# Kernel tuning notes

Measured on AMD Instinct MI355X. Metric: run time of the kernel, lower is better.

Reference implementation:

```python
import jax, jax.numpy as jnp
import numpy as np
import math

G = 128          # graphs per batch
N_PER = 512      # nodes per graph (equal-size, contiguous layout)
N = G * N_PER    # 65536 nodes
DEG = 16
E = N * DEG      # 1,048,576 edges
IN_C, HID, OUT_C = 100, 128, 2
RATIO = 0.8
EPS = 1e-5

K1 = int(math.ceil(RATIO * N_PER))  # 410
K2 = int(math.ceil(RATIO * K1))     # 328
K3 = int(math.ceil(RATIO * K2))     # 263


def gcn_conv(x, src, dst, emask, W, b):
    # GCNConv: linear, symmetric deg^-1/2 norm with self-loops, scatter-add
    xl = x @ W
    n = x.shape[0]
    w = emask.astype(x.dtype)
    deg = jnp.ones((n,), x.dtype).at[dst].add(w)      # +1 from self loop
    dinv = jax.lax.rsqrt(deg)
    coef = dinv[src] * dinv[dst] * w                  # [E]
    out = jnp.zeros_like(xl).at[dst].add(coef[:, None] * xl[src])
    out = out + (dinv * dinv)[:, None] * xl           # self-loop messages
    return out + b


def batch_norm(x, gamma, beta):
    # BatchNorm1d over node dim (training-mode batch statistics)
    mu = x.mean(0)
    var = x.var(0)
    return (x - mu) * jax.lax.rsqrt(var + EPS) * gamma + beta


def topk_pool(x, src, dst, emask, att, g, n, k):
    # TopKPooling: score = tanh(x@att/||att||), keep top-k per graph, gate features,
    # drop edges touching removed nodes (via validity mask).
    score = jnp.tanh((x @ att) / jnp.linalg.norm(att))
    _, idx = jax.lax.top_k(score.reshape(g, n), k)           # [g,k] local ids
    kept = (idx + (jnp.arange(g) * n)[:, None]).reshape(-1)   # global ids
    new_x = x[kept] * score[kept][:, None]
    old2new = jnp.full((g * n,), -1, jnp.int32).at[kept].set(
        jnp.arange(g * k, dtype=jnp.int32))
    s2, d2 = old2new[src], old2new[dst]
    valid = emask & (s2 >= 0) & (d2 >= 0)
    return new_x, jnp.maximum(s2, 0), jnp.maximum(d2, 0), valid


def readout(x, g, k):
    # [global_max_pool, global_mean_pool] over each graph's k nodes
    xr = x.reshape(g, k, -1)
    return jnp.concatenate([xr.max(1), xr.mean(1)], axis=1)   # [g, 2C]


def setup_inputs() -> dict:
    key = jax.random.key(0)
    ks = jax.random.split(key, 16)
    x = jax.random.normal(ks[0], (N, IN_C), jnp.float32)
    # within-graph random edges, then offset by graph id
    e_per = E // G
    local = jax.random.randint(ks[1], (2, G, e_per), 0, N_PER)
    edge_index = (local + (jnp.arange(G) * N_PER)[None, :, None]).reshape(2, E).astype(jnp.int32)
    batch = jnp.repeat(jnp.arange(G, dtype=jnp.int32), N_PER)

    def w(k, fi, fo):
        return jax.random.normal(k, (fi, fo), jnp.float32) * (1.0 / np.sqrt(fi))

    z = lambda c: jnp.zeros((c,), jnp.float32)
    o = lambda c: jnp.ones((c,), jnp.float32)
    return {
        'x': x, 'edge_index': edge_index, 'batch': batch,
        'Wp': w(ks[2], IN_C, 128), 'bp': z(128),
        'W1': w(ks[3], 128, HID), 'b1': z(HID), 'g1': o(HID), 'be1': z(HID),
        'att1': jax.random.normal(ks[4], (HID,), jnp.float32),
        'W2': w(ks[5], HID, HID), 'b2': z(HID), 'g2': o(HID), 'be2': z(HID),
        'att2': jax.random.normal(ks[6], (HID,), jnp.float32),
        'W3': w(ks[7], HID, HID), 'b3': z(HID), 'g3': o(HID), 'be3': z(HID),
        'att3': jax.random.normal(ks[8], (HID,), jnp.float32),
        'Wl1': w(ks[9], 2 * HID, HID), 'bl1': z(HID),
        'Wl2': w(ks[10], HID, OUT_C), 'bl2': z(OUT_C),
    }


def reference(x, edge_index, batch, Wp, bp, W1, b1, g1, be1, att1,
              W2, b2, g2, be2, att2, W3, b3, g3, be3, att3,
              Wl1, bl1, Wl2, bl2):
    src, dst = edge_index[0], edge_index[1]
    emask = jnp.ones((E,), bool)
    h = jax.nn.relu(x @ Wp + bp)

    h = jax.nn.relu(batch_norm(gcn_conv(h, src, dst, emask, W1, b1), g1, be1))
    h, src, dst, emask = topk_pool(h, src, dst, emask, att1, G, N_PER, K1)
    x1 = readout(h, G, K1)

    h = jax.nn.relu(batch_norm(gcn_conv(h, src, dst, emask, W2, b2), g2, be2))
    h, src, dst, emask = topk_pool(h, src, dst, emask, att2, G, K1, K2)
    x2 = readout(h, G, K2)

    h = jax.nn.relu(batch_norm(gcn_conv(h, src, dst, emask, W3, b3), g3, be3))
    h, src, dst, emask = topk_pool(h, src, dst, emask, att3, G, K2, K3)
    x3 = readout(h, G, K3)

    s = x1 + x2 + x3                       # [G, 2*HID]
    s = jax.nn.relu(s @ Wl1 + bl1)
    return s @ Wl2 + bl2                   # [G, OUT_C]
```

## Files before the change

### kernel.cpp

```cpp
#include <hip/hip_runtime.h>
#include <math.h>

#define G     128
#define NPER  512
#define NTOT  65536
#define E_TOT 1048576
#define EPG   8192
#define INC   100
#define HID   128
#define KP1   410
#define KP2   328
#define KP3   263

__global__ void init_kernel(short* __restrict__ cmap, float* __restrict__ sread,
                            float* __restrict__ bnpart) {
    int t = blockIdx.x * 256 + threadIdx.x;
    if (t < NTOT) cmap[t] = (short)(t & (NPER - 1));
    if (t < G * 256) sread[t] = 0.f;
    if (t < 3 * G * 256) bnpart[t] = 0.f;
}

__global__ __launch_bounds__(512, 2) void csr_build0(
    const int* __restrict__ src, const int* __restrict__ dst,
    unsigned short* __restrict__ csr_g, int* __restrict__ rowptr_g)
{
    __shared__ int cnt_s[NPER];
    __shared__ int rowptr_s[NPER + 1];
    __shared__ int wo_s[NPER];
    __shared__ int chunksum_s[9];

    const int g = blockIdx.x, tid = threadIdx.x, lane = tid & 63, wv = tid >> 6;
    const int ebase = g * EPG, obase = g * NPER;

    cnt_s[tid] = 0;
    __syncthreads();
    for (int e = tid; e < EPG; e += 512)
        atomicAdd(&cnt_s[dst[ebase + e] - obase], 1);
    __syncthreads();

    int v = cnt_s[tid], x = v;
#pragma unroll
    for (int d = 1; d < 64; d <<= 1) {
        int y = __shfl_up(x, d);
        if (lane >= d) x += y;
    }
    if (lane == 63) chunksum_s[wv] = x;
    __syncthreads();
    if (tid == 0) {
        int acc = 0;
#pragma unroll
        for (int k = 0; k < 8; ++k) { int t = chunksum_s[k]; chunksum_s[k] = acc; acc += t; }
    }
    __syncthreads();
    int excl = x - v + chunksum_s[wv];
    rowptr_s[tid] = excl; wo_s[tid] = excl;
    if (tid == 511) rowptr_s[512] = excl + v;
    __syncthreads();

    for (int i = tid; i <= NPER; i += 512) rowptr_g[g * 513 + i] = rowptr_s[i];
    for (int e = tid; e < EPG; e += 512) {
        int sl = src[ebase + e] - obase, dl = dst[ebase + e] - obase;
        int pos = atomicAdd(&wo_s[dl], 1);
        csr_g[g * EPG + pos] = (unsigned short)sl;
    }
}

__global__ __launch_bounds__(256, 2) void gemm_pre(
    const float* __restrict__ A, const float* __restrict__ W,
    const float* __restrict__ bias, float* __restrict__ out, int M)
{
    constexpr int K = INC, KC = 32;
    __shared__ float Ws[KC][128];
    __shared__ float As[KC][132];
    const int tid  = threadIdx.x;
    const int row0 = blockIdx.x * 128;
    const int r0 = (tid >> 4) * 8;
    const int c0 = (tid & 15) * 8;

    float acc[8][8];
#pragma unroll
    for (int i = 0; i < 8; ++i)
#pragma unroll
        for (int j = 0; j < 8; ++j) acc[i][j] = 0.f;

    for (int k0 = 0; k0 < K; k0 += KC) {
        const int kc  = (K - k0 < KC) ? (K - k0) : KC;
        const int nf4 = kc >> 2;

        for (int i = tid; i < kc * 32; i += 256) {
            int kk = i >> 5, c4 = i & 31;
            *((float4*)&Ws[kk][0] + c4) =
                *((const float4*)(W + (size_t)(k0 + kk) * 128) + c4);
        }
        for (int i = tid; i < nf4 * 128; i += 256) {
            int row = i / nf4, f4 = i - row * nf4;
            float4 v = *(const float4*)(A + (size_t)(row0 + row) * K + k0 + f4 * 4);
            As[f4 * 4 + 0][row] = v.x;
            As[f4 * 4 + 1][row] = v.y;
            As[f4 * 4 + 2][row] = v.z;
            As[f4 * 4 + 3][row] = v.w;
        }
        __syncthreads();

#pragma unroll 4
        for (int kk = 0; kk < kc; ++kk) {
            float4 b0 = *(const float4*)&Ws[kk][c0];
            float4 b1 = *(const float4*)&Ws[kk][c0 + 4];
            float4 a0 = *(const float4*)&As[kk][r0];
            float4 a1 = *(const float4*)&As[kk][r0 + 4];
            float a[8] = {a0.x, a0.y, a0.z, a0.w, a1.x, a1.y, a1.z, a1.w};
            float b[8] = {b0.x, b0.y, b0.z, b0.w, b1.x, b1.y, b1.z, b1.w};
#pragma unroll
            for (int i = 0; i < 8; ++i)
#pragma unroll
                for (int j = 0; j < 8; ++j)
                    acc[i][j] += a[i] * b[j];
        }
        __syncthreads();
    }

#pragma unroll
    for (int i = 0; i < 8; ++i) {
        int row = row0 + r0 + i;
        float o[8];
#pragma unroll
        for (int j = 0; j < 8; ++j)
            o[j] = fmaxf(acc[i][j] + bias[c0 + j], 0.f);
        float* po = out + (size_t)row * 128 + c0;
        *(float4*)po       = make_float4(o[0], o[1], o[2], o[3]);
        *(float4*)(po + 4) = make_float4(o[4], o[5], o[6], o[7]);
    }
}

template<int NCUR>
__global__ __launch_bounds__(256, 2) void gemm128(
    const float* __restrict__ A, const float* __restrict__ W,
    const int* __restrict__ rowptr_g, float* __restrict__ out)
{
    constexpr int KC = 32;
    __shared__ float Ws[2][KC][128];
    __shared__ float As[2][KC][132];
    __shared__ float dinv_ls[128];
    const int tid  = threadIdx.x;
    const int row0 = blockIdx.x * 128;
    const int r0 = (tid >> 4) * 8;
    const int c0 = (tid & 15) * 8;

    if (tid < 128) {
        int row = row0 + tid;
        int gg = row / NCUR, ll = row - gg * NCUR;
        const int* rp = rowptr_g + gg * 513 + ll;
        dinv_ls[tid] = rsqrtf((float)(rp[1] - rp[0] + 1));
    }

    const float4* W4 = (const float4*)W;

#pragma unroll
    for (int j = 0; j < 4; ++j) {
        int i = tid + j * 256;
        int kk = i >> 5, c4 = i & 31;
        *((float4*)&Ws[0][kk][0] + c4) = W4[kk * 32 + c4];
    }
#pragma unroll
    for (int j = 0; j < 4; ++j) {
        int i = tid + j * 256;
        int row = i >> 3, f4 = i & 7;
        float4 v = *(const float4*)(A + (size_t)(row0 + row) * 128 + f4 * 4);
        As[0][f4 * 4 + 0][row] = v.x;
        As[0][f4 * 4 + 1][row] = v.y;
        As[0][f4 * 4 + 2][row] = v.z;
        As[0][f4 * 4 + 3][row] = v.w;
    }
    __syncthreads();

    float acc[8][8];
#pragma unroll
    for (int i = 0; i < 8; ++i)
#pragma unroll
        for (int j = 0; j < 8; ++j) acc[i][j] = 0.f;

    int p = 0;
    for (int k0 = 0; k0 < 128; k0 += KC) {
        const int kn = k0 + KC;
        const bool has = kn < 128;

        float4 wreg[4], areg[4];
        if (has) {
#pragma unroll
            for (int j = 0; j < 4; ++j) {
                int i = tid + j * 256;
                int kk = i >> 5, c4 = i & 31;
                wreg[j] = W4[(kn + kk) * 32 + c4];
            }
#pragma unroll
            for (int j = 0; j < 4; ++j) {
                int i = tid + j * 256;
                int row = i >> 3, f4 = i & 7;
                areg[j] = *(const float4*)(A + (size_t)(row0 + row) * 128 + kn + f4 * 4);
            }
        }

#pragma unroll 4
        for (int kk = 0; kk < KC; ++kk) {
            float4 b0 = *(const float4*)&Ws[p][kk][c0];
            float4 b1 = *(const float4*)&Ws[p][kk][c0 + 4];
            float4 a0 = *(const float4*)&As[p][kk][r0];
            float4 a1 = *(const float4*)&As[p][kk][r0 + 4];
            float a[8] = {a0.x, a0.y, a0.z, a0.w, a1.x, a1.y, a1.z, a1.w};
            float b[8] = {b0.x, b0.y, b0.z, b0.w, b1.x, b1.y, b1.z, b1.w};
#pragma unroll
            for (int i = 0; i < 8; ++i)
#pragma unroll
                for (int j = 0; j < 8; ++j)
                    acc[i][j] += a[i] * b[j];
        }

        if (has) {
            int q = p ^ 1;
#pragma unroll
            for (int j = 0; j < 4; ++j) {
                int i = tid + j * 256;
                int kk = i >> 5, c4 = i & 31;
                *((float4*)&Ws[q][kk][0] + c4) = wreg[j];
            }
#pragma unroll
            for (int j = 0; j < 4; ++j) {
                int i = tid + j * 256;
                int row = i >> 3, f4 = i & 7;
                float4 v = areg[j];
                As[q][f4 * 4 + 0][row] = v.x;
                As[q][f4 * 4 + 1][row] = v.y;
                As[q][f4 * 4 + 2][row] = v.z;
                As[q][f4 * 4 + 3][row] = v.w;
            }
        }
        __syncthreads();
        p ^= 1;
    }

#pragma unroll
    for (int i = 0; i < 8; ++i) {
        int row = row0 + r0 + i;
        float dv = dinv_ls[r0 + i];
        float o[8];
#pragma unroll
        for (int j = 0; j < 8; ++j) o[j] = acc[i][j] * dv;
        float* po = out + (size_t)row * 128 + c0;
        *(float4*)po       = make_float4(o[0], o[1], o[2], o[3]);
        *(float4*)(po + 4) = make_float4(o[4], o[5], o[6], o[7]);
    }
}

template<int NCUR>
__global__ __launch_bounds__(256, 8) void gather_kernel(
    const float* __restrict__ xs, const unsigned short* __restrict__ csr_g,
    const int* __restrict__ rowptr_g, const float* __restrict__ bvec,
    float* __restrict__ out, float* __restrict__ bnpart)
{
    constexpr int CHUNK = (NCUR + 15) / 16;
    constexpr int CSRCAP = 1536;
    __shared__ int   rowptr_s[CHUNK + 1];
    __shared__ unsigned short csr_s[CSRCAP];
    __shared__ float red_s[512];

    const int g = blockIdx.x, s = blockIdx.y;
    const int tid = threadIdx.x, lane = tid & 63, w = tid >> 6;
    const int nbase = g * NCUR;
    const int d0 = s * CHUNK;
    const int d1 = (d0 + CHUNK < NCUR) ? d0 + CHUNK : NCUR;
    const int len = d1 - d0;

    const int* rp = rowptr_g + g * 513 + d0;
    for (int i = tid; i <= len; i += 256) rowptr_s[i] = rp[i];
    __syncthreads();

    const int base = rowptr_s[0];
    int nume = rowptr_s[len] - base;
    if (nume > CSRCAP) nume = CSRCAP;
    const unsigned short* cg = csr_g + g * EPG + base;
    for (int i = tid; i < nume; i += 256) csr_s[i] = cg[i];
    __syncthreads();

    const float2* x2g = (const float2*)xs + (size_t)nbase * 64 + lane;
    float2* o2p = (float2*)out;
    const float2 b2 = ((const float2*)bvec)[lane];
    float2 sum = make_float2(0.f, 0.f), sq = make_float2(0.f, 0.f);

    for (int da = d0 + w; da < d1; da += 8) {
        const int db = da + 4;
        const bool hb = db < d1;
        const int ra = da - d0, rb = db - d0;
        const int ia = rowptr_s[ra] - base;
        const int na = rowptr_s[ra + 1] - rowptr_s[ra];
        const int ib = hb ? rowptr_s[rb] - base : 0;
        const int nbl = hb ? rowptr_s[rb + 1] - rowptr_s[rb] : 0;
        const float dva = rsqrtf((float)(na + 1));
        const float dvb = rsqrtf((float)(nbl + 1));

        float2 accA = x2g[(size_t)da * 64];
        float2 accB = make_float2(0.f, 0.f);
        if (hb) accB = x2g[(size_t)db * 64];

        const int nmin = na < nbl ? na : nbl;
#pragma unroll 2
        for (int t = 0; t < nmin; ++t) {
            int sa = csr_s[ia + t], sb = csr_s[ib + t];
            float2 va = x2g[(size_t)sa * 64];
            float2 vb = x2g[(size_t)sb * 64];
            accA.x += va.x; accA.y += va.y;
            accB.x += vb.x; accB.y += vb.y;
        }
#pragma unroll 4
        for (int t = nmin; t < na; ++t) {
            float2 va = x2g[(size_t)csr_s[ia + t] * 64];
            accA.x += va.x; accA.y += va.y;
        }
#pragma unroll 4
        for (int t = nmin; t < nbl; ++t) {
            float2 vb = x2g[(size_t)csr_s[ib + t] * 64];
            accB.x += vb.x; accB.y += vb.y;
        }

        float2 oA = make_float2(b2.x + dva * accA.x, b2.y + dva * accA.y);
        o2p[(size_t)(nbase + da) * 64 + lane] = oA;
        sum.x += oA.x; sum.y += oA.y;
        sq.x  += oA.x * oA.x; sq.y += oA.y * oA.y;
        if (hb) {
            float2 oB = make_float2(b2.x + dvb * accB.x, b2.y + dvb * accB.y);
            o2p[(size_t)(nbase + db) * 64 + lane] = oB;
            sum.x += oB.x; sum.y += oB.y;
            sq.x  += oB.x * oB.x; sq.y += oB.y * oB.y;
        }
    }

    float2* red2 = (float2*)red_s;
    red2[tid] = sum; __syncthreads();
    if (tid < 64) {
        float2 a = red2[tid], b_ = red2[tid + 64],
               c = red2[tid + 128], d_ = red2[tid + 192];
        atomicAdd(&bnpart[g * 256 + 2 * tid],     a.x + b_.x + c.x + d_.x);
        atomicAdd(&bnpart[g * 256 + 2 * tid + 1], a.y + b_.y + c.y + d_.y);
    }
    __syncthreads();
    red2[tid] = sq; __syncthreads();
    if (tid < 64) {
        float2 a = red2[tid], b_ = red2[tid + 64],
               c = red2[tid + 128], d_ = red2[tid + 192];
        atomicAdd(&bnpart[g * 256 + 128 + 2 * tid],     a.x + b_.x + c.x + d_.x);
        atomicAdd(&bnpart[g * 256 + 128 + 2 * tid + 1], a.y + b_.y + c.y + d_.y);
    }
}

__global__ __launch_bounds__(1024, 1) void bnfin_kernel(
    const float* __restrict__ bnpart, float n,
    const float* __restrict__ gamma, const float* __restrict__ beta,
    const float* __restrict__ att, float* __restrict__ coefs)
{
    __shared__ float ssum[8][128];
    __shared__ float ssq[8][128];
    __shared__ float r[128];
    const int t = threadIdx.x & 127, slice = threadIdx.x >> 7;
    float s = 0.f, q = 0.f;
    for (int g = slice; g < G; g += 8) {
        s += bnpart[g * 256 + t];
        q += bnpart[g * 256 + 128 + t];
    }
    ssum[slice][t] = s; ssq[slice][t] = q;
    if (threadIdx.x < 128) { float av = att[t]; r[t] = av * av; }
    __syncthreads();
    if (threadIdx.x < 128) {
        float S = 0.f, Q = 0.f;
#pragma unroll
        for (int k = 0; k < 8; ++k) { S += ssum[k][t]; Q += ssq[k][t]; }
        for (int st = 64; st > 0; st >>= 1) {
            if (t < st) r[t] += r[t + st];
            __syncthreads();
        }
        float norm = sqrtf(r[0]);
        float mu   = S / n;
        float var  = Q / n - mu * mu;
        float inv  = rsqrtf(var + 1e-5f);
        float a    = gamma[t] * inv;
        coefs[t]        = a;
        coefs[128 + t]  = beta[t] - mu * a;
        coefs[256 + t]  = att[t] / norm;
    }
}

template<int NCUR, int KK, bool BUILD>
__global__ __launch_bounds__(1024, 1) void pool_kernel(
    const float* __restrict__ gcn, const float* __restrict__ coefs,
    float* __restrict__ newx, short* __restrict__ cmap,
    float* __restrict__ sread,
    const int* __restrict__ src, const int* __restrict__ dst,
    unsigned short* __restrict__ csr_g, int* __restrict__ rowptr_g)
{
    __shared__ float score_s[NCUR];
    __shared__ unsigned long long key_s[NCUR];
    __shared__ short o2n_s[NCUR];
    __shared__ unsigned short n2o_s[KK];
    __shared__ short cmap_s[NPER];
    __shared__ float2 red2[1024];
    __shared__ int   cnt_s[512];
    __shared__ int   rowptr_s[513];
    __shared__ int   wo_s[512];
    __shared__ int   chunksum_s[9];

    const int g = blockIdx.x, tid = threadIdx.x, lane = tid & 63, w = tid >> 6;
    const int nb = g * NCUR;
    const int ebase = g * EPG, obase = g * NPER;
    const float a0 = coefs[lane],       a1 = coefs[64 + lane];
    const float c0 = coefs[128 + lane], c1 = coefs[192 + lane];
    const float t0 = coefs[256 + lane], t1 = coefs[320 + lane];

    for (int i = tid; i < NPER; i += 1024) cmap_s[i] = cmap[obase + i];

    for (int i = w; i < NCUR; i += 16) {
        const float* row = gcn + (size_t)(nb + i) * 128;
        float h0 = fmaxf(a0 * row[lane] + c0, 0.f);
        float h1 = fmaxf(a1 * row[64 + lane] + c1, 0.f);
        float p  = h0 * t0 + h1 * t1;
#pragma unroll
        for (int off = 32; off > 0; off >>= 1) p += __shfl_down(p, off);
        if (lane == 0) score_s[i] = tanhf(p);
    }
    __syncthreads();

    for (int i = tid; i < NCUR; i += 1024) {
        unsigned u   = __float_as_uint(score_s[i]);
        unsigned key = (u & 0x80000000u) ? ~u : (u | 0x80000000u);
        key_s[i] = ((unsigned long long)key << 32) |
                   (unsigned long long)(0xFFFFFFFFu - (unsigned)i);
    }
    __syncthreads();

    for (int i = tid; i < NCUR; i += 1024) {
        const unsigned long long ki = key_s[i];
        int r = 0;
#pragma unroll 8
        for (int j = 0; j < NCUR; ++j) r += (key_s[j] > ki) ? 1 : 0;
        o2n_s[i] = (r < KK) ? (short)r : (short)-1;
        if (r < KK) n2o_s[r] = (unsigned short)i;
    }
    __syncthreads();

    float mx0 = -1e30f, mx1 = -1e30f, sm0 = 0.f, sm1 = 0.f;
    for (int j2 = w; j2 < KK; j2 += 16) {
        int old = n2o_s[j2];
        float s = score_s[old];
        const float* row = gcn + (size_t)(nb + old) * 128;
        float h0 = fmaxf(a0 * row[lane] + c0, 0.f) * s;
        float h1 = fmaxf(a1 * row[64 + lane] + c1, 0.f) * s;
        float* orow = newx + (size_t)(g * KK + j2) * 128;
        orow[lane]      = h0;
        orow[64 + lane] = h1;
        mx0 = fmaxf(mx0, h0); mx1 = fmaxf(mx1, h1);
        sm0 += h0; sm1 += h1;
    }
    red2[tid] = make_float2(mx0, mx1);
    __syncthreads();
    if (tid < 64) {
        float m = -1e30f;
#pragma unroll
        for (int w2 = 0; w2 < 16; ++w2) m = fmaxf(m, red2[w2 * 64 + tid].x);
        sread[g * 256 + tid] += m;
    } else if (tid < 128) {
        int l = tid - 64;
        float m = -1e30f;
#pragma unroll
        for (int w2 = 0; w2 < 16; ++w2) m = fmaxf(m, red2[w2 * 64 + l].y);
        sread[g * 256 + tid] += m;
    }
    __syncthreads();
    red2[tid] = make_float2(sm0, sm1);
    __syncthreads();
    if (tid < 64) {
        float sm = 0.f;
#pragma unroll
        for (int w2 = 0; w2 < 16; ++w2) sm += red2[w2 * 64 + tid].x;
        sread[g * 256 + 128 + tid] += sm * (1.0f / KK);
    } else if (tid < 128) {
        int l = tid - 64;
        float sm = 0.f;
#pragma unroll
        for (int w2 = 0; w2 < 16; ++w2) sm += red2[w2 * 64 + l].y;
        sread[g * 256 + 128 + tid] += sm * (1.0f / KK);
    }

    for (int o = tid; o < NPER; o += 1024) {
        int m = cmap_s[o];
        short nm = (m >= 0) ? o2n_s[m] : (short)-1;
        cmap_s[o] = nm;
        cmap[obase + o] = nm;
    }

    if (!BUILD) return;
    __syncthreads();

    if (tid < 512) cnt_s[tid] = 0;
    __syncthreads();
    for (int e = tid; e < EPG; e += 1024) {
        int sl = cmap_s[src[ebase + e] - obase];
        int dl = cmap_s[dst[ebase + e] - obase];
        if ((sl | dl) >= 0) atomicAdd(&cnt_s[dl], 1);
    }
    __syncthreads();
    int v = 0, x = 0;
    if (tid < 512) {
        v = cnt_s[tid]; x = v;
#pragma unroll
        for (int d = 1; d < 64; d <<= 1) {
            int y = __shfl_up(x, d);
            if (lane >= d) x += y;
        }
        if (lane == 63) chunksum_s[w] = x;
    }
    __syncthreads();
    if (tid == 0) {
        int acc = 0;
#pragma unroll
        for (int k = 0; k < 8; ++k) { int t = chunksum_s[k]; chunksum_s[k] = acc; acc += t; }
    }
    __syncthreads();
    if (tid < 512) {
        int excl = x - v + chunksum_s[w];
        rowptr_s[tid] = excl; wo_s[tid] = excl;
        if (tid == 511) rowptr_s[512] = excl + v;
    }
    __syncthreads();
    for (int i = tid; i <= 512; i += 1024) rowptr_g[g * 513 + i] = rowptr_s[i];
    for (int e = tid; e < EPG; e += 1024) {
        int sl = cmap_s[src[ebase + e] - obase];
        int dl = cmap_s[dst[ebase + e] - obase];
        if ((sl | dl) >= 0) {
            int pos = atomicAdd(&wo_s[dl], 1);
            csr_g[g * EPG + pos] = (unsigned short)sl;
        }
    }
}

__global__ void final_kernel(const float* __restrict__ sread,
                             const float* __restrict__ Wl1,
                             const float* __restrict__ bl1,
                             const float* __restrict__ Wl2,
                             const float* __restrict__ bl2,
                             float* __restrict__ out)
{
    __shared__ float s_s[256];
    __shared__ float hid_s[128];
    int g = blockIdx.x, t = threadIdx.x;
    s_s[t]       = sread[g * 256 + t];
    s_s[128 + t] = sread[g * 256 + 128 + t];
    __syncthreads();
    float acc = bl1[t];
    for (int i = 0; i < 256; ++i) acc += s_s[i] * Wl1[i * 128 + t];
    hid_s[t] = fmaxf(acc, 0.f);
    __syncthreads();
    if (t < 2) {
        float o = bl2[t];
        for (int j = 0; j < 128; ++j) o += hid_s[j] * Wl2[j * 2 + t];
        out[g * 2 + t] = o;
    }
}

extern "C" void kernel_launch(void* const* d_in, const int* in_sizes, int n_in,
                              void* d_out, int out_size, void* d_ws, size_t ws_size,
                              hipStream_t stream)
{
    const float* x    = (const float*)d_in[0];
    const int*   ei   = (const int*)d_in[1];
    const float* Wp   = (const float*)d_in[3];
    const float* bp   = (const float*)d_in[4];
    const float* W1   = (const float*)d_in[5];
    const float* b1   = (const float*)d_in[6];
    const float* g1   = (const float*)d_in[7];
    const float* be1  = (const float*)d_in[8];
    const float* att1 = (const float*)d_in[9];
    const float* W2   = (const float*)d_in[10];
    const float* b2   = (const float*)d_in[11];
    const float* g2   = (const float*)d_in[12];
    const float* be2  = (const float*)d_in[13];
    const float* att2 = (const float*)d_in[14];
    const float* W3   = (const float*)d_in[15];
    const float* b3   = (const float*)d_in[16];
    const float* g3   = (const float*)d_in[17];
    const float* be3  = (const float*)d_in[18];
    const float* att3 = (const float*)d_in[19];
    const float* Wl1  = (const float*)d_in[20];
    const float* bl1  = (const float*)d_in[21];
    const float* Wl2  = (const float*)d_in[22];
    const float* bl2  = (const float*)d_in[23];
    float* out = (float*)d_out;

    const int* srcp = ei;
    const int* dstp = ei + E_TOT;

    char* ws = (char*)d_ws;
    float*          bufA   = (float*)ws;
    float*          bufB   = (float*)(ws + 33554432);
    unsigned short* csr    = (unsigned short*)(ws + 67108864);
    int*            rowptr = (int*)  (ws + 69206016);
    float*          bnpart = (float*)(ws + 69468672);
    short*          cmap   = (short*)(ws + 69861888);
    float*          sread  = (float*)(ws + 69992960);
    float*          coefs  = (float*)(ws + 70124032);

    float* bn0 = bnpart;
    float* bn1 = bnpart + G * 256;
    float* bn2 = bnpart + 2 * G * 256;

    init_kernel<<<384, 256, 0, stream>>>(cmap, sread, bnpart);
    csr_build0<<<G, 512, 0, stream>>>(srcp, dstp, csr, rowptr);

    gemm_pre<<<512, 256, 0, stream>>>(x, Wp, bp, bufA, NTOT);

    gemm128<NPER><<<512, 256, 0, stream>>>(bufA, W1, rowptr, bufB);
    gather_kernel<NPER><<<dim3(G, 16), 256, 0, stream>>>(bufB, csr, rowptr, b1, bufA, bn0);
    bnfin_kernel<<<1, 1024, 0, stream>>>(bn0, (float)NTOT, g1, be1, att1, coefs);
    pool_kernel<NPER, KP1, true><<<G, 1024, 0, stream>>>(
        bufA, coefs, bufB, cmap, sread, srcp, dstp, csr, rowptr);

    gemm128<KP1><<<410, 256, 0, stream>>>(bufB, W2, rowptr, bufA);
    gather_kernel<KP1><<<dim3(G, 16), 256, 0, stream>>>(bufA, csr, rowptr, b2, bufB, bn1);
    bnfin_kernel<<<1, 1024, 0, stream>>>(bn1, (float)(G * KP1), g2, be2, att2, coefs);
    pool_kernel<KP1, KP2, true><<<G, 1024, 0, stream>>>(
        bufB, coefs, bufA, cmap, sread, srcp, dstp, csr, rowptr);

    gemm128<KP2><<<328, 256, 0, stream>>>(bufA, W3, rowptr, bufB);
    gather_kernel<KP2><<<dim3(G, 16), 256, 0, stream>>>(bufB, csr, rowptr, b3, bufA, bn2);
    bnfin_kernel<<<1, 1024, 0, stream>>>(bn2, (float)(G * KP2), g3, be3, att3, coefs);
    pool_kernel<KP2, KP3, false><<<G, 1024, 0, stream>>>(
        bufA, coefs, bufB, cmap, sread, srcp, dstp, csr, rowptr);

    final_kernel<<<G, 128, 0, stream>>>(sread, Wl1, bl1, Wl2, bl2, out);
}
```

Baseline: 485.6 us.

## Split pool kernel into parallel score, select and gate kernels

Each per-graph pool kernel ran as 128 blocks of 1024 threads. It is now split into three kernels. The score and gating/readout kernels each launch 1024 smaller blocks to spread the memory-bound row reads across more CUs. Only the top-k ranking and CSR rebuild stay per-graph. The readout max and mean are accumulated with global atomics, the max using an order-preserving uint encoding, and the last stage skips writing gated features that are never read. In exchange there are extra launches, a global round trip for scores and the n2o map, and atomic contention on the readout buffers.

```diff
diff --git a/kernel.cpp b/kernel.cpp
--- a/kernel.cpp
+++ b/kernel.cpp
@@ -12,12 +12,21 @@
 #define KP2   328
 #define KP3   263
 
-__global__ void init_kernel(short* __restrict__ cmap, float* __restrict__ sread,
-                            float* __restrict__ bnpart) {
+__device__ __forceinline__ unsigned encf(float x) {
+    unsigned u = __float_as_uint(x);
+    return (u & 0x80000000u) ? ~u : (u | 0x80000000u);
+}
+__device__ __forceinline__ float decf(unsigned e) {
+    return (e & 0x80000000u) ? __uint_as_float(e ^ 0x80000000u)
+                             : __uint_as_float(~e);
+}
+
+__global__ void init_kernel(short* __restrict__ cmap, float* __restrict__ bnpart,
+                            unsigned* __restrict__ rmax, float* __restrict__ rsum) {
     int t = blockIdx.x * 256 + threadIdx.x;
     if (t < NTOT) cmap[t] = (short)(t & (NPER - 1));
-    if (t < G * 256) sread[t] = 0.f;
     if (t < 3 * G * 256) bnpart[t] = 0.f;
+    if (t < 3 * G * 128) { rmax[t] = 0u; rsum[t] = 0.f; }
 }
 
 __global__ __launch_bounds__(512, 2) void csr_build0(
@@ -387,20 +396,43 @@
     }
 }
 
+template<int NCUR>
+__global__ __launch_bounds__(256, 8) void score_kernel(
+    const float* __restrict__ gcn, const float* __restrict__ coefs,
+    float* __restrict__ score_g)
+{
+    constexpr int CHUNK = (NCUR + 7) / 8;
+    const int g = blockIdx.x, s = blockIdx.y;
+    const int tid = threadIdx.x, lane = tid & 63, w = tid >> 6;
+    const int nb = g * NCUR;
+    const int i0 = s * CHUNK;
+    const int i1 = (i0 + CHUNK < NCUR) ? i0 + CHUNK : NCUR;
+
+    const float a0 = coefs[lane],       a1 = coefs[64 + lane];
+    const float c0 = coefs[128 + lane], c1 = coefs[192 + lane];
+    const float t0 = coefs[256 + lane], t1 = coefs[320 + lane];
+
+    for (int i = i0 + w; i < i1; i += 4) {
+        const float* row = gcn + (size_t)(nb + i) * 128;
+        float h0 = fmaxf(a0 * row[lane] + c0, 0.f);
+        float h1 = fmaxf(a1 * row[64 + lane] + c1, 0.f);
+        float p  = h0 * t0 + h1 * t1;
+#pragma unroll
+        for (int off = 32; off > 0; off >>= 1) p += __shfl_down(p, off);
+        if (lane == 0) score_g[nb + i] = tanhf(p);
+    }
+}
+
 template<int NCUR, int KK, bool BUILD>
-__global__ __launch_bounds__(1024, 1) void pool_kernel(
-    const float* __restrict__ gcn, const float* __restrict__ coefs,
-    float* __restrict__ newx, short* __restrict__ cmap,
-    float* __restrict__ sread,
+__global__ __launch_bounds__(1024, 1) void select_kernel(
+    const float* __restrict__ score_g, short* __restrict__ cmap,
+    unsigned short* __restrict__ n2o_g,
     const int* __restrict__ src, const int* __restrict__ dst,
     unsigned short* __restrict__ csr_g, int* __restrict__ rowptr_g)
 {
-    __shared__ float score_s[NCUR];
     __shared__ unsigned long long key_s[NCUR];
     __shared__ short o2n_s[NCUR];
-    __shared__ unsigned short n2o_s[KK];
     __shared__ short cmap_s[NPER];
-    __shared__ float2 red2[1024];
     __shared__ int   cnt_s[512];
     __shared__ int   rowptr_s[513];
     __shared__ int   wo_s[512];
@@ -409,25 +441,10 @@
     const int g = blockIdx.x, tid = threadIdx.x, lane = tid & 63, w = tid >> 6;
     const int nb = g * NCUR;
     const int ebase = g * EPG, obase = g * NPER;
-    const float a0 = coefs[lane],       a1 = coefs[64 + lane];
-    const float c0 = coefs[128 + lane], c1 = coefs[192 + lane];
-    const float t0 = coefs[256 + lane], t1 = coefs[320 + lane];
 
     for (int i = tid; i < NPER; i += 1024) cmap_s[i] = cmap[obase + i];
-
-    for (int i = w; i < NCUR; i += 16) {
-        const float* row = gcn + (size_t)(nb + i) * 128;
-        float h0 = fmaxf(a0 * row[lane] + c0, 0.f);
-        float h1 = fmaxf(a1 * row[64 + lane] + c1, 0.f);
-        float p  = h0 * t0 + h1 * t1;
-#pragma unroll
-        for (int off = 32; off > 0; off >>= 1) p += __shfl_down(p, off);
-        if (lane == 0) score_s[i] = tanhf(p);
-    }
-    __syncthreads();
-
     for (int i = tid; i < NCUR; i += 1024) {
-        unsigned u   = __float_as_uint(score_s[i]);
+        unsigned u   = __float_as_uint(score_g[nb + i]);
         unsigned key = (u & 0x80000000u) ? ~u : (u | 0x80000000u);
         key_s[i] = ((unsigned long long)key << 32) |
                    (unsigned long long)(0xFFFFFFFFu - (unsigned)i);
@@ -440,52 +457,9 @@
 #pragma unroll 8
         for (int j = 0; j < NCUR; ++j) r += (key_s[j] > ki) ? 1 : 0;
         o2n_s[i] = (r < KK) ? (short)r : (short)-1;
-        if (r < KK) n2o_s[r] = (unsigned short)i;
-    }
-    __syncthreads();
-
-    float mx0 = -1e30f, mx1 = -1e30f, sm0 = 0.f, sm1 = 0.f;
-    for (int j2 = w; j2 < KK; j2 += 16) {
-        int old = n2o_s[j2];
-        float s = score_s[old];
-        const float* row = gcn + (size_t)(nb + old) * 128;
-        float h0 = fmaxf(a0 * row[lane] + c0, 0.f) * s;
-        float h1 = fmaxf(a1 * row[64 + lane] + c1, 0.f) * s;
-        float* orow = newx + (size_t)(g * KK + j2) * 128;
-        orow[lane]      = h0;
-        orow[64 + lane] = h1;
-        mx0 = fmaxf(mx0, h0); mx1 = fmaxf(mx1, h1);
-        sm0 += h0; sm1 += h1;
-    }
-    red2[tid] = make_float2(mx0, mx1);
-    __syncthreads();
-    if (tid < 64) {
-        float m = -1e30f;
-#pragma unroll
-        for (int w2 = 0; w2 < 16; ++w2) m = fmaxf(m, red2[w2 * 64 + tid].x);
-        sread[g * 256 + tid] += m;
-    } else if (tid < 128) {
-        int l = tid - 64;
-        float m = -1e30f;
-#pragma unroll
-        for (int w2 = 0; w2 < 16; ++w2) m = fmaxf(m, red2[w2 * 64 + l].y);
-        sread[g * 256 + tid] += m;
-    }
-    __syncthreads();
-    red2[tid] = make_float2(sm0, sm1);
-    __syncthreads();
-    if (tid < 64) {
-        float sm = 0.f;
-#pragma unroll
-        for (int w2 = 0; w2 < 16; ++w2) sm += red2[w2 * 64 + tid].x;
-        sread[g * 256 + 128 + tid] += sm * (1.0f / KK);
-    } else if (tid < 128) {
-        int l = tid - 64;
-        float sm = 0.f;
-#pragma unroll
-        for (int w2 = 0; w2 < 16; ++w2) sm += red2[w2 * 64 + l].y;
-        sread[g * 256 + 128 + tid] += sm * (1.0f / KK);
-    }
+        if (r < KK) n2o_g[g * 512 + r] = (unsigned short)i;
+    }
+    __syncthreads();
 
     for (int o = tid; o < NPER; o += 1024) {
         int m = cmap_s[o];
@@ -539,7 +513,62 @@
     }
 }
 
-__global__ void final_kernel(const float* __restrict__ sread,
+template<int NCUR, int KK, bool STORE>
+__global__ __launch_bounds__(256, 8) void gate_kernel(
+    const float* __restrict__ gcn, const float* __restrict__ coefs,
+    const float* __restrict__ score_g, const unsigned short* __restrict__ n2o_g,
+    float* __restrict__ newx, unsigned* __restrict__ rmax,
+    float* __restrict__ rsum)
+{
+    constexpr int CHUNK = (KK + 7) / 8;
+    __shared__ float2 red2[256];
+    const int g = blockIdx.x, s = blockIdx.y;
+    const int tid = threadIdx.x, lane = tid & 63, w = tid >> 6;
+    const int nb = g * NCUR;
+    const int j0 = s * CHUNK;
+    const int j1 = (j0 + CHUNK < KK) ? j0 + CHUNK : KK;
+
+    const float a0 = coefs[lane],       a1 = coefs[64 + lane];
+    const float c0 = coefs[128 + lane], c1 = coefs[192 + lane];
+
+    float mx0 = -1e30f, mx1 = -1e30f, sm0 = 0.f, sm1 = 0.f;
+    for (int j2 = j0 + w; j2 < j1; j2 += 4) {
+        int old = n2o_g[g * 512 + j2];
+        float sc = score_g[nb + old];
+        const float* row = gcn + (size_t)(nb + old) * 128;
+        float h0 = fmaxf(a0 * row[lane] + c0, 0.f) * sc;
+        float h1 = fmaxf(a1 * row[64 + lane] + c1, 0.f) * sc;
+        if (STORE) {
+            float* orow = newx + (size_t)(g * KK + j2) * 128;
+            orow[lane]      = h0;
+            orow[64 + lane] = h1;
+        }
+        mx0 = fmaxf(mx0, h0); mx1 = fmaxf(mx1, h1);
+        sm0 += h0; sm1 += h1;
+    }
+    red2[tid] = make_float2(mx0, mx1);
+    __syncthreads();
+    if (tid < 64) {
+        float m0 = fmaxf(fmaxf(red2[tid].x, red2[tid + 64].x),
+                         fmaxf(red2[tid + 128].x, red2[tid + 192].x));
+        float m1 = fmaxf(fmaxf(red2[tid].y, red2[tid + 64].y),
+                         fmaxf(red2[tid + 128].y, red2[tid + 192].y));
+        atomicMax(&rmax[g * 128 + tid],      encf(m0));
+        atomicMax(&rmax[g * 128 + 64 + tid], encf(m1));
+    }
+    __syncthreads();
+    red2[tid] = make_float2(sm0, sm1);
+    __syncthreads();
+    if (tid < 64) {
+        float s0 = red2[tid].x + red2[tid + 64].x + red2[tid + 128].x + red2[tid + 192].x;
+        float s1 = red2[tid].y + red2[tid + 64].y + red2[tid + 128].y + red2[tid + 192].y;
+        atomicAdd(&rsum[g * 128 + tid],      s0);
+        atomicAdd(&rsum[g * 128 + 64 + tid], s1);
+    }
+}
+
+__global__ void final_kernel(const unsigned* __restrict__ rmax,
+                             const float* __restrict__ rsum,
                              const float* __restrict__ Wl1,
                              const float* __restrict__ bl1,
                              const float* __restrict__ Wl2,
@@ -549,8 +578,12 @@
     __shared__ float s_s[256];
     __shared__ float hid_s[128];
     int g = blockIdx.x, t = threadIdx.x;
-    s_s[t]       = sread[g * 256 + t];
-    s_s[128 + t] = sread[g * 256 + 128 + t];
+    s_s[t] = decf(rmax[g * 128 + t]) +
+             decf(rmax[G * 128 + g * 128 + t]) +
+             decf(rmax[2 * G * 128 + g * 128 + t]);
+    s_s[128 + t] = rsum[g * 128 + t] * (1.0f / KP1) +
+                   rsum[G * 128 + g * 128 + t] * (1.0f / KP2) +
+                   rsum[2 * G * 128 + g * 128 + t] * (1.0f / KP3);
     __syncthreads();
     float acc = bl1[t];
     for (int i = 0; i < 256; ++i) acc += s_s[i] * Wl1[i * 128 + t];
@@ -596,20 +629,27 @@
     const int* dstp = ei + E_TOT;
 
     char* ws = (char*)d_ws;
-    float*          bufA   = (float*)ws;
-    float*          bufB   = (float*)(ws + 33554432);
-    unsigned short* csr    = (unsigned short*)(ws + 67108864);
-    int*            rowptr = (int*)  (ws + 69206016);
-    float*          bnpart = (float*)(ws + 69468672);
-    short*          cmap   = (short*)(ws + 69861888);
-    float*          sread  = (float*)(ws + 69992960);
-    float*          coefs  = (float*)(ws + 70124032);
+    float*          bufA    = (float*)ws;
+    float*          bufB    = (float*)(ws + 33554432);
+    unsigned short* csr     = (unsigned short*)(ws + 67108864);
+    int*            rowptr  = (int*)  (ws + 69206016);
+    float*          bnpart  = (float*)(ws + 69468672);
+    short*          cmap    = (short*)(ws + 69861888);
+    float*          score_g = (float*)(ws + 69992960);
+    unsigned short* n2o     = (unsigned short*)(ws + 70255104);
+    unsigned*       rmax    = (unsigned*)(ws + 70386176);
+    float*          rsum    = (float*)(ws + 70582784);
+    float*          coefs   = (float*)(ws + 70779392);
 
     float* bn0 = bnpart;
     float* bn1 = bnpart + G * 256;
     float* bn2 = bnpart + 2 * G * 256;
-
-    init_kernel<<<384, 256, 0, stream>>>(cmap, sread, bnpart);
+    unsigned* rmax0 = rmax,            * rmax1 = rmax + G * 128, * rmax2 = rmax + 2 * G * 128;
+    float*    rsum0 = rsum;
+    float*    rsum1 = rsum + G * 128;
+    float*    rsum2 = rsum + 2 * G * 128;
+
+    init_kernel<<<384, 256, 0, stream>>>(cmap, bnpart, rmax, rsum);
     csr_build0<<<G, 512, 0, stream>>>(srcp, dstp, csr, rowptr);
 
     gemm_pre<<<512, 256, 0, stream>>>(x, Wp, bp, bufA, NTOT);
@@ -617,20 +657,29 @@
     gemm128<NPER><<<512, 256, 0, stream>>>(bufA, W1, rowptr, bufB);
     gather_kernel<NPER><<<dim3(G, 16), 256, 0, stream>>>(bufB, csr, rowptr, b1, bufA, bn0);
     bnfin_kernel<<<1, 1024, 0, stream>>>(bn0, (float)NTOT, g1, be1, att1, coefs);
-    pool_kernel<NPER, KP1, true><<<G, 1024, 0, stream>>>(
-        bufA, coefs, bufB, cmap, sread, srcp, dstp, csr, rowptr);
+    score_kernel<NPER><<<dim3(G, 8), 256, 0, stream>>>(bufA, coefs, score_g);
+    select_kernel<NPER, KP1, true><<<G, 1024, 0, stream>>>(
+        score_g, cmap, n2o, srcp, dstp, csr, rowptr);
+    gate_kernel<NPER, KP1, true><<<dim3(G, 8), 256, 0, stream>>>(
+        bufA, coefs, score_g, n2o, bufB, rmax0, rsum0);
 
     gemm128<KP1><<<410, 256, 0, stream>>>(bufB, W2, rowptr, bufA);
     gather_kernel<KP1><<<dim3(G, 16), 256, 0, stream>>>(bufA, csr, rowptr, b2, bufB, bn1);
     bnfin_kernel<<<1, 1024, 0, stream>>>(bn1, (float)(G * KP1), g2, be2, att2, coefs);
-    pool_kernel<KP1, KP2, true><<<G, 1024, 0, stream>>>(
-        bufB, coefs, bufA, cmap, sread, srcp, dstp, csr, rowptr);
+    score_kernel<KP1><<<dim3(G, 8), 256, 0, stream>>>(bufB, coefs, score_g);
+    select_kernel<KP1, KP2, true><<<G, 1024, 0, stream>>>(
+        score_g, cmap, n2o, srcp, dstp, csr, rowptr);
+    gate_kernel<KP1, KP2, true><<<dim3(G, 8), 256, 0, stream>>>(
+        bufB, coefs, score_g, n2o, bufA, rmax1, rsum1);
 
     gemm128<KP2><<<328, 256, 0, stream>>>(bufA, W3, rowptr, bufB);
     gather_kernel<KP2><<<dim3(G, 16), 256, 0, stream>>>(bufB, csr, rowptr, b3, bufA, bn2);
     bnfin_kernel<<<1, 1024, 0, stream>>>(bn2, (float)(G * KP2), g3, be3, att3, coefs);
-    pool_kernel<KP2, KP3, false><<<G, 1024, 0, stream>>>(
-        bufA, coefs, bufB, cmap, sread, srcp, dstp, csr, rowptr);
-
-    final_kernel<<<G, 128, 0, stream>>>(sread, Wl1, bl1, Wl2, bl2, out);
-}
+    score_kernel<KP2><<<dim3(G, 8), 256, 0, stream>>>(bufA, coefs, score_g);
+    select_kernel<KP2, KP3, false><<<G, 1024, 0, stream>>>(
+        score_g, cmap, n2o, srcp, dstp, csr, rowptr);
+    gate_kernel<KP2, KP3, false><<<dim3(G, 8), 256, 0, stream>>>(
+        bufA, coefs, score_g, n2o, nullptr, rmax2, rsum2);
+
+    final_kernel<<<G, 128, 0, stream>>>(rmax, rsum, Wl1, bl1, Wl2, bl2, out);
+}
```

New measurement: 486.5 us. Within noise of the previous version (+0.2%).
